# Kernel optimization log

Measured on AMD Instinct MI355X. Metric: run time of the kernel, lower is better.

## Reference

```python
import jax, jax.numpy as jnp
import numpy as np

N_NODES = 100000
N_EDGES = 1600000
H_FEATS = 128
OUT_CLASSES = 6


def setup_inputs() -> dict:
    key = jax.random.key(0)
    ks = jax.random.split(key, 9)
    h = jax.random.normal(ks[0], (N_NODES, H_FEATS), dtype=jnp.float32)
    src = jax.random.randint(ks[1], (N_EDGES,), 0, N_NODES)
    dst = jax.random.randint(ks[2], (N_EDGES,), 0, N_NODES)
    # torch nn.Linear convention: y = x @ W.T + b, W shape [out, in]
    W1 = jax.random.normal(ks[3], (64, 2 * H_FEATS), dtype=jnp.float32) * 0.05
    b1 = jax.random.normal(ks[4], (64,), dtype=jnp.float32) * 0.05
    W2 = jax.random.normal(ks[5], (32, 64), dtype=jnp.float32) * 0.05
    b2 = jax.random.normal(ks[6], (32,), dtype=jnp.float32) * 0.05
    W3 = jax.random.normal(ks[7], (OUT_CLASSES, 32), dtype=jnp.float32) * 0.05
    b3 = jax.random.normal(ks[8], (OUT_CLASSES,), dtype=jnp.float32) * 0.05
    return {"h": h, "src": src, "dst": dst, "W1": W1, "b1": b1,
            "W2": W2, "b2": b2, "W3": W3, "b3": b3}


def reference(h, src, dst, W1, b1, W2, b2, W3, b3):
    # Per-edge gather of src/dst node features, concat -> [E, 2*H]
    x = jnp.concatenate([h[src], h[dst]], axis=1)
    x = jax.nn.relu(x @ W1.T + b1)   # [E, 64]
    x = jax.nn.relu(x @ W2.T + b2)   # [E, 32]
    return x @ W3.T + b3             # [E, output_class]
```

## Files before the change

kernel.cpp:

```cpp
#include <hip/hip_runtime.h>
#include <hip/hip_bf16.h>
#include <stdint.h>


#define H 128

typedef short bf16x8 __attribute__((ext_vector_type(8)));
typedef float f32x4  __attribute__((ext_vector_type(4)));

__device__ __forceinline__ uint16_t f2bf(float f) {
    uint32_t u = __float_as_uint(f);
    return (uint16_t)((u + 0x7fffu + ((u >> 16) & 1u)) >> 16);
}

__device__ __forceinline__ uint32_t cvtpk(float lo, float hi) {
    uint32_t r;
    asm("v_cvt_pk_bf16_f32 %0, %1, %2" : "=v"(r) : "v"(lo), "v"(hi));
    return r;
}

__device__ __forceinline__ uint32_t bfadd2_relu(uint32_t a, uint32_t b) {
    float alo = __uint_as_float(a << 16);
    float ahi = __uint_as_float(a & 0xffff0000u);
    float blo = __uint_as_float(b << 16);
    float bhi = __uint_as_float(b & 0xffff0000u);
    float slo = fmaxf(alo + blo, 0.f);
    float shi = fmaxf(ahi + bhi, 0.f);
    return cvtpk(slo, shi);
}

__global__ void prep_weights(const float* __restrict__ W1,
                             const float* __restrict__ W2,
                             const float* __restrict__ W3,
                             uint16_t* __restrict__ Bfrag,
                             uint16_t* __restrict__ EFrag)
{
    int t = blockIdx.x * blockDim.x + threadIdx.x;
    int stride = gridDim.x * blockDim.x;
    for (int i = t; i < 4 * 8 * 64 * 8; i += stride) {
        int j    = i & 7;
        int lane = (i >> 3) & 63;
        int nt   = (i >> 9) & 7;
        int kt   = (i >> 12);
        int k = kt * 32 + (lane >> 4) * 8 + j;
        int n = nt * 16 + (lane & 15);
        float v = (n < 64) ? W1[n * 256 + k] : W1[(n - 64) * 256 + 128 + k];
        Bfrag[i] = f2bf(v);
    }
    for (int i = t; i < 5 * 64 * 8; i += stride) {
        int j    = i & 7;
        int lane = (i >> 3) & 63;
        int f    = i >> 9;
        uint16_t v;
        if (f < 4) {
            int kt = f >> 1, nt = f & 1;
            int k = kt * 32 + (lane >> 4) * 8 + j;
            int n = nt * 16 + (lane & 15);
            v = f2bf(W2[n * 64 + k]);
        } else {
            int k = (lane >> 4) * 8 + j;
            int n = lane & 15;
            v = (n < 6) ? f2bf(W3[n * 32 + k]) : (uint16_t)0;
        }
        EFrag[i] = v;
    }
}

__global__ void __launch_bounds__(256) node_gemm(
    const float* __restrict__ h,
    const uint16_t* __restrict__ Bfrag,
    const float* __restrict__ b1,
    uint16_t* __restrict__ pre, int N)
{
    const int wave = threadIdx.x >> 6;
    const int lane = threadIdx.x & 63;
    const int n0 = (blockIdx.x * 4 + wave) * 32;
    if (n0 >= N) return;

    const int m15  = lane & 15;
    const int quad = lane >> 4;

    bf16x8 hb[2][4];
#pragma unroll
    for (int t = 0; t < 2; t++) {
        int row = n0 + t * 16 + m15; if (row >= N) row = N - 1;
        const float* hrow = h + (size_t)row * H + quad * 8;
#pragma unroll
        for (int kt = 0; kt < 4; kt++) {
            float4 lo = *(const float4*)(hrow + kt * 32);
            float4 hi = *(const float4*)(hrow + kt * 32 + 4);
            union { bf16x8 v; uint32_t u[4]; } B;
            B.u[0] = cvtpk(lo.x, lo.y); B.u[1] = cvtpk(lo.z, lo.w);
            B.u[2] = cvtpk(hi.x, hi.y); B.u[3] = cvtpk(hi.z, hi.w);
            hb[t][kt] = B.v;
        }
    }

    const bool ok0 = (n0 + m15) < N;
    const bool ok1 = (n0 + 16 + m15) < N;
    uint16_t* prow0 = pre + (size_t)(n0 + m15) * H;
    uint16_t* prow1 = pre + (size_t)(n0 + 16 + m15) * H;

#pragma unroll
    for (int ct = 0; ct < 8; ct++) {
        f32x4 acc0 = {0.f, 0.f, 0.f, 0.f};
        f32x4 acc1 = {0.f, 0.f, 0.f, 0.f};
#pragma unroll
        for (int kt = 0; kt < 4; kt++) {
            bf16x8 afr = *(const bf16x8*)(Bfrag + ((size_t)(kt * 8 + ct) * 64 + lane) * 8);
            acc0 = __builtin_amdgcn_mfma_f32_16x16x32_bf16(afr, hb[0][kt], acc0, 0, 0, 0);
            acc1 = __builtin_amdgcn_mfma_f32_16x16x32_bf16(afr, hb[1][kt], acc1, 0, 0, 0);
        }
        float4 bv = {0.f, 0.f, 0.f, 0.f};
        if (ct < 4) bv = *(const float4*)(b1 + ct * 16 + quad * 4);
        const int off = ct * 16 + quad * 4;
        if (ok0) {
            uint32_t p0 = cvtpk(acc0[0] + bv.x, acc0[1] + bv.y);
            uint32_t p1 = cvtpk(acc0[2] + bv.z, acc0[3] + bv.w);
            *(uint2*)(prow0 + off) = uint2{p0, p1};
        }
        if (ok1) {
            uint32_t p0 = cvtpk(acc1[0] + bv.x, acc1[1] + bv.y);
            uint32_t p1 = cvtpk(acc1[2] + bv.z, acc1[3] + bv.w);
            *(uint2*)(prow1 + off) = uint2{p0, p1};
        }
    }
}

__global__ void __launch_bounds__(256) edge_mlp(
    const uint16_t* __restrict__ pre,
    const int* __restrict__ src, const int* __restrict__ dst,
    const uint16_t* __restrict__ EFrag,
    const float* __restrict__ b2, const float* __restrict__ b3,
    float* __restrict__ out, long E)
{
    __shared__ uint16_t zbuf[4][64 * 40];

    const int wave = threadIdx.x >> 6;
    const int lane = threadIdx.x & 63;
    const int m15  = lane & 15;
    const int quad = lane >> 4;
    uint16_t* zw = &zbuf[wave][0];

    const long e0 = (long)(blockIdx.x * 4 + wave) * 64;
    if (e0 >= E) return;

    long ea = e0 + m15;
    long eb = (ea + 16 < E) ? ea + 16 : E - 1;
    long ec = (ea + 32 < E) ? ea + 32 : E - 1;
    long ed = (ea + 48 < E) ? ea + 48 : E - 1;
    if (ea >= E) ea = E - 1;
    int sa = src[ea], da = dst[ea];
    int sb = src[eb], db = dst[eb];
    int sc = src[ec], dc = dst[ec];
    int sd = src[ed], dd = dst[ed];

    bf16x8 bL2[4], bL3;
#pragma unroll
    for (int f = 0; f < 4; f++) bL2[f] = *(const bf16x8*)(EFrag + (f * 64 + lane) * 8);
    bL3 = *(const bf16x8*)(EFrag + (4 * 64 + lane) * 8);
    const float4 vb2a4 = *(const float4*)(b2 + quad * 4);
    const float4 vb2b4 = *(const float4*)(b2 + 16 + quad * 4);
    const float vb3  = (m15 < 6) ? b3[m15] : 0.f;

    const char* preb = (const char*)pre;
    const uint32_t qo = (uint32_t)quad * 16u;
    uint32_t oa0 = (uint32_t)sa * 256u + qo,        ob0 = (uint32_t)da * 256u + 128u + qo;
    uint32_t oa1 = (uint32_t)sb * 256u + qo,        ob1 = (uint32_t)db * 256u + 128u + qo;
    uint32_t oa2 = (uint32_t)sc * 256u + qo,        ob2 = (uint32_t)dc * 256u + 128u + qo;
    uint32_t oa3 = (uint32_t)sd * 256u + qo,        ob3 = (uint32_t)dd * 256u + 128u + qo;

    uint4 a00 = *(const uint4*)(preb + oa0);
    uint4 a01 = *(const uint4*)(preb + oa0 + 64);
    uint4 b00 = *(const uint4*)(preb + ob0);
    uint4 b01 = *(const uint4*)(preb + ob0 + 64);
    uint4 a10 = *(const uint4*)(preb + oa1);
    uint4 a11 = *(const uint4*)(preb + oa1 + 64);
    uint4 b10 = *(const uint4*)(preb + ob1);
    uint4 b11 = *(const uint4*)(preb + ob1 + 64);
    uint4 a20 = *(const uint4*)(preb + oa2);
    uint4 a21 = *(const uint4*)(preb + oa2 + 64);
    uint4 b20 = *(const uint4*)(preb + ob2);
    uint4 b21 = *(const uint4*)(preb + ob2 + 64);
    uint4 a30 = *(const uint4*)(preb + oa3);
    uint4 a31 = *(const uint4*)(preb + oa3 + 64);
    uint4 b30 = *(const uint4*)(preb + ob3);
    uint4 b31 = *(const uint4*)(preb + ob3 + 64);

    __builtin_amdgcn_sched_barrier(0);

#define DO_SUBTILE(ST, UA0, UB0, UA1, UB1)                                        \
    {                                                                             \
        union { bf16x8 v; uint32_t u[4]; } A0, A1;                                \
        A0.u[0] = bfadd2_relu(UA0.x, UB0.x);                                      \
        A0.u[1] = bfadd2_relu(UA0.y, UB0.y);                                      \
        A0.u[2] = bfadd2_relu(UA0.z, UB0.z);                                      \
        A0.u[3] = bfadd2_relu(UA0.w, UB0.w);                                      \
        A1.u[0] = bfadd2_relu(UA1.x, UB1.x);                                      \
        A1.u[1] = bfadd2_relu(UA1.y, UB1.y);                                      \
        A1.u[2] = bfadd2_relu(UA1.z, UB1.z);                                      \
        A1.u[3] = bfadd2_relu(UA1.w, UB1.w);                                      \
        _Pragma("unroll")                                                         \
        for (int nt = 0; nt < 2; nt++) {                                          \
            f32x4 acc = {0.f, 0.f, 0.f, 0.f};                                     \
            acc = __builtin_amdgcn_mfma_f32_16x16x32_bf16(bL2[nt], A0.v, acc, 0, 0, 0); \
            acc = __builtin_amdgcn_mfma_f32_16x16x32_bf16(bL2[2 + nt], A1.v, acc, 0, 0, 0); \
            const float4 bv = nt ? vb2b4 : vb2a4;                                 \
            uint32_t p0 = cvtpk(fmaxf(acc[0] + bv.x, 0.f), fmaxf(acc[1] + bv.y, 0.f)); \
            uint32_t p1 = cvtpk(fmaxf(acc[2] + bv.z, 0.f), fmaxf(acc[3] + bv.w, 0.f)); \
            *(uint2*)(zw + ((ST) * 16 + m15) * 40 + nt * 16 + quad * 4) = uint2{p0, p1}; \
        }                                                                         \
    }

    DO_SUBTILE(0, a00, b00, a01, b01)
    DO_SUBTILE(1, a10, b10, a11, b11)
    DO_SUBTILE(2, a20, b20, a21, b21)
    DO_SUBTILE(3, a30, b30, a31, b31)
#undef DO_SUBTILE

#pragma unroll
    for (int st = 0; st < 4; st++) {
        bf16x8 a3 = *(const bf16x8*)(zw + (st * 16 + m15) * 40 + quad * 8);
        f32x4 o = {0.f, 0.f, 0.f, 0.f};
        o = __builtin_amdgcn_mfma_f32_16x16x32_bf16(a3, bL3, o, 0, 0, 0);
        if (m15 < 6) {
#pragma unroll
            for (int r = 0; r < 4; r++) {
                long e = e0 + st * 16 + quad * 4 + r;
                if (e < E) out[e * 6 + m15] = o[r] + vb3;
            }
        }
    }
}

extern "C" void kernel_launch(void* const* d_in, const int* in_sizes, int n_in,
                              void* d_out, int out_size, void* d_ws, size_t ws_size,
                              hipStream_t stream) {
    const float* h   = (const float*)d_in[0];
    const int*   src = (const int*)d_in[1];
    const int*   dst = (const int*)d_in[2];
    const float* W1  = (const float*)d_in[3];
    const float* b1  = (const float*)d_in[4];
    const float* W2  = (const float*)d_in[5];
    const float* b2  = (const float*)d_in[6];
    const float* W3  = (const float*)d_in[7];
    const float* b3  = (const float*)d_in[8];

    const int  N = in_sizes[0] / H;
    const long E = in_sizes[1];

    char* ws = (char*)d_ws;
    uint16_t* Bfrag = (uint16_t*)ws;
    uint16_t* EFrag = (uint16_t*)(ws + 64 * 1024);
    uint16_t* pre   = (uint16_t*)(ws + 128 * 1024);

    prep_weights<<<64, 256, 0, stream>>>(W1, W2, W3, Bfrag, EFrag);
    node_gemm<<<(N + 127) / 128, 256, 0, stream>>>(h, Bfrag, b1, pre, N);
    const int eblocks = (int)((E + 255) / 256);
    edge_mlp<<<eblocks, 256, 0, stream>>>(pre, src, dst, EFrag, b2, b3,
                                          (float*)d_out, E);
}
```

Baseline: 188.2 us.

## Coalesce pre-activation gathers per row and pipeline loads with manual vmcnt waits

```diff
diff --git a/kernel.cpp b/kernel.cpp
--- a/kernel.cpp
+++ b/kernel.cpp
@@ -7,6 +7,7 @@
 
 typedef short bf16x8 __attribute__((ext_vector_type(8)));
 typedef float f32x4  __attribute__((ext_vector_type(4)));
+typedef uint32_t u32x4 __attribute__((ext_vector_type(4)));
 
 __device__ __forceinline__ uint16_t f2bf(float f) {
     uint32_t u = __float_as_uint(f);
@@ -127,6 +128,14 @@
     }
 }
 
+#define GLOAD(dst, off)   asm volatile("global_load_dwordx4 %0, %1, %2"           \
+                                       : "=v"(dst) : "v"(off), "s"(preb))
+#define GLOAD64(dst, off) asm volatile("global_load_dwordx4 %0, %1, %2 offset:64" \
+                                       : "=v"(dst) : "v"(off), "s"(preb))
+#define VMWAIT(N) do { asm volatile("s_waitcnt vmcnt(" #N ")" ::: "memory");      \
+                       __builtin_amdgcn_sched_barrier(0); } while (0)
+#define LAUNDER(x) asm volatile("" : "+v"(x))
+
 __global__ void __launch_bounds__(256) edge_mlp(
     const uint16_t* __restrict__ pre,
     const int* __restrict__ src, const int* __restrict__ dst,
@@ -140,83 +149,91 @@
     const int lane = threadIdx.x & 63;
     const int m15  = lane & 15;
     const int quad = lane >> 4;
+    const int em   = lane >> 2;
+    const int ch4  = lane & 3;
     uint16_t* zw = &zbuf[wave][0];
 
     const long e0 = (long)(blockIdx.x * 4 + wave) * 64;
     if (e0 >= E) return;
 
-    long ea = e0 + m15;
-    long eb = (ea + 16 < E) ? ea + 16 : E - 1;
-    long ec = (ea + 32 < E) ? ea + 32 : E - 1;
-    long ed = (ea + 48 < E) ? ea + 48 : E - 1;
-    if (ea >= E) ea = E - 1;
-    int sa = src[ea], da = dst[ea];
-    int sb = src[eb], db = dst[eb];
-    int sc = src[ec], dc = dst[ec];
-    int sd = src[ed], dd = dst[ed];
-
+    uint32_t oa[4], ob[4];
+#pragma unroll
+    for (int st = 0; st < 4; st++) {
+        long e = e0 + st * 16 + em;
+        if (e >= E) e = E - 1;
+        oa[st] = (uint32_t)src[e] * 256u + (uint32_t)ch4 * 16u;
+        ob[st] = (uint32_t)dst[e] * 256u + 128u + (uint32_t)ch4 * 16u;
+    }
     bf16x8 bL2[4], bL3;
 #pragma unroll
     for (int f = 0; f < 4; f++) bL2[f] = *(const bf16x8*)(EFrag + (f * 64 + lane) * 8);
     bL3 = *(const bf16x8*)(EFrag + (4 * 64 + lane) * 8);
-    const float4 vb2a4 = *(const float4*)(b2 + quad * 4);
-    const float4 vb2b4 = *(const float4*)(b2 + 16 + quad * 4);
-    const float vb3  = (m15 < 6) ? b3[m15] : 0.f;
+    float4 t2a = *(const float4*)(b2 + quad * 4);
+    float4 t2b = *(const float4*)(b2 + 16 + quad * 4);
+    float ba0 = t2a.x, ba1 = t2a.y, ba2 = t2a.z, ba3 = t2a.w;
+    float bb0 = t2b.x, bb1 = t2b.y, bb2 = t2b.z, bb3 = t2b.w;
+    float vb3 = (m15 < 6) ? b3[m15] : 0.f;
+
+    LAUNDER(bL2[0]); LAUNDER(bL2[1]); LAUNDER(bL2[2]); LAUNDER(bL2[3]); LAUNDER(bL3);
+    LAUNDER(ba0); LAUNDER(ba1); LAUNDER(ba2); LAUNDER(ba3);
+    LAUNDER(bb0); LAUNDER(bb1); LAUNDER(bb2); LAUNDER(bb3); LAUNDER(vb3);
+    asm volatile("s_waitcnt vmcnt(0)" ::: "memory");
+    __builtin_amdgcn_sched_barrier(0);
 
     const char* preb = (const char*)pre;
-    const uint32_t qo = (uint32_t)quad * 16u;
-    uint32_t oa0 = (uint32_t)sa * 256u + qo,        ob0 = (uint32_t)da * 256u + 128u + qo;
-    uint32_t oa1 = (uint32_t)sb * 256u + qo,        ob1 = (uint32_t)db * 256u + 128u + qo;
-    uint32_t oa2 = (uint32_t)sc * 256u + qo,        ob2 = (uint32_t)dc * 256u + 128u + qo;
-    uint32_t oa3 = (uint32_t)sd * 256u + qo,        ob3 = (uint32_t)dd * 256u + 128u + qo;
-
-    uint4 a00 = *(const uint4*)(preb + oa0);
-    uint4 a01 = *(const uint4*)(preb + oa0 + 64);
-    uint4 b00 = *(const uint4*)(preb + ob0);
-    uint4 b01 = *(const uint4*)(preb + ob0 + 64);
-    uint4 a10 = *(const uint4*)(preb + oa1);
-    uint4 a11 = *(const uint4*)(preb + oa1 + 64);
-    uint4 b10 = *(const uint4*)(preb + ob1);
-    uint4 b11 = *(const uint4*)(preb + ob1 + 64);
-    uint4 a20 = *(const uint4*)(preb + oa2);
-    uint4 a21 = *(const uint4*)(preb + oa2 + 64);
-    uint4 b20 = *(const uint4*)(preb + ob2);
-    uint4 b21 = *(const uint4*)(preb + ob2 + 64);
-    uint4 a30 = *(const uint4*)(preb + oa3);
-    uint4 a31 = *(const uint4*)(preb + oa3 + 64);
-    uint4 b30 = *(const uint4*)(preb + ob3);
-    uint4 b31 = *(const uint4*)(preb + ob3 + 64);
-
-    __builtin_amdgcn_sched_barrier(0);
-
-#define DO_SUBTILE(ST, UA0, UB0, UA1, UB1)                                        \
+    const int bp = ((m15 << 2) | quad) << 2;
+
+    u32x4 s0g0, s0g1, s0g2, s0g3, s1g0, s1g1, s1g2, s1g3;
+    u32x4 s2g0, s2g1, s2g2, s2g3, s3g0, s3g1, s3g2, s3g3;
+
+#define ISSUE(ST)                                                                 \
+    GLOAD  (s##ST##g0, oa[ST]);                   \
+    GLOAD64(s##ST##g1, oa[ST]);                   \
+    GLOAD  (s##ST##g2, ob[ST]);                   \
+    GLOAD64(s##ST##g3, ob[ST]);
+
+#define COMPUTE(ST)                                                               \
     {                                                                             \
-        union { bf16x8 v; uint32_t u[4]; } A0, A1;                                \
-        A0.u[0] = bfadd2_relu(UA0.x, UB0.x);                                      \
-        A0.u[1] = bfadd2_relu(UA0.y, UB0.y);                                      \
-        A0.u[2] = bfadd2_relu(UA0.z, UB0.z);                                      \
-        A0.u[3] = bfadd2_relu(UA0.w, UB0.w);                                      \
-        A1.u[0] = bfadd2_relu(UA1.x, UB1.x);                                      \
-        A1.u[1] = bfadd2_relu(UA1.y, UB1.y);                                      \
-        A1.u[2] = bfadd2_relu(UA1.z, UB1.z);                                      \
-        A1.u[3] = bfadd2_relu(UA1.w, UB1.w);                                      \
+        u32x4 Y0, Y1;                                                             \
+        Y0.x = bfadd2_relu(s##ST##g0.x, s##ST##g2.x);                             \
+        Y0.y = bfadd2_relu(s##ST##g0.y, s##ST##g2.y);                             \
+        Y0.z = bfadd2_relu(s##ST##g0.z, s##ST##g2.z);                             \
+        Y0.w = bfadd2_relu(s##ST##g0.w, s##ST##g2.w);                             \
+        Y1.x = bfadd2_relu(s##ST##g1.x, s##ST##g3.x);                             \
+        Y1.y = bfadd2_relu(s##ST##g1.y, s##ST##g3.y);                             \
+        Y1.z = bfadd2_relu(s##ST##g1.z, s##ST##g3.z);                             \
+        Y1.w = bfadd2_relu(s##ST##g1.w, s##ST##g3.w);                             \
+        union { bf16x8 v; int u[4]; } A0, A1;                                     \
+        A0.u[0] = __builtin_amdgcn_ds_bpermute(bp, (int)Y0.x);                    \
+        A0.u[1] = __builtin_amdgcn_ds_bpermute(bp, (int)Y0.y);                    \
+        A0.u[2] = __builtin_amdgcn_ds_bpermute(bp, (int)Y0.z);                    \
+        A0.u[3] = __builtin_amdgcn_ds_bpermute(bp, (int)Y0.w);                    \
+        A1.u[0] = __builtin_amdgcn_ds_bpermute(bp, (int)Y1.x);                    \
+        A1.u[1] = __builtin_amdgcn_ds_bpermute(bp, (int)Y1.y);                    \
+        A1.u[2] = __builtin_amdgcn_ds_bpermute(bp, (int)Y1.z);                    \
+        A1.u[3] = __builtin_amdgcn_ds_bpermute(bp, (int)Y1.w);                    \
         _Pragma("unroll")                                                         \
         for (int nt = 0; nt < 2; nt++) {                                          \
             f32x4 acc = {0.f, 0.f, 0.f, 0.f};                                     \
             acc = __builtin_amdgcn_mfma_f32_16x16x32_bf16(bL2[nt], A0.v, acc, 0, 0, 0); \
             acc = __builtin_amdgcn_mfma_f32_16x16x32_bf16(bL2[2 + nt], A1.v, acc, 0, 0, 0); \
-            const float4 bv = nt ? vb2b4 : vb2a4;                                 \
-            uint32_t p0 = cvtpk(fmaxf(acc[0] + bv.x, 0.f), fmaxf(acc[1] + bv.y, 0.f)); \
-            uint32_t p1 = cvtpk(fmaxf(acc[2] + bv.z, 0.f), fmaxf(acc[3] + bv.w, 0.f)); \
+            const float c0 = nt ? bb0 : ba0, c1 = nt ? bb1 : ba1;                 \
+            const float c2 = nt ? bb2 : ba2, c3 = nt ? bb3 : ba3;                 \
+            uint32_t p0 = cvtpk(fmaxf(acc[0] + c0, 0.f), fmaxf(acc[1] + c1, 0.f)); \
+            uint32_t p1 = cvtpk(fmaxf(acc[2] + c2, 0.f), fmaxf(acc[3] + c3, 0.f)); \
             *(uint2*)(zw + ((ST) * 16 + m15) * 40 + nt * 16 + quad * 4) = uint2{p0, p1}; \
         }                                                                         \
     }
 
-    DO_SUBTILE(0, a00, b00, a01, b01)
-    DO_SUBTILE(1, a10, b10, a11, b11)
-    DO_SUBTILE(2, a20, b20, a21, b21)
-    DO_SUBTILE(3, a30, b30, a31, b31)
-#undef DO_SUBTILE
+    ISSUE(0) ISSUE(1)
+    ISSUE(2)
+    VMWAIT(8);  COMPUTE(0)
+    ISSUE(3)
+    VMWAIT(8);  COMPUTE(1)
+    VMWAIT(4);  COMPUTE(2)
+    VMWAIT(0);  COMPUTE(3)
+#undef ISSUE
+#undef COMPUTE
 
 #pragma unroll
     for (int st = 0; st < 4; st++) {
```

Result: faster. 184.0 us (-2.3%).
